# Kernel optimization log

Hardware: AMD Instinct MI355X
Metric: run time of the kernel (lower is better)

Reference implementation:

```python
import jax, jax.numpy as jnp
import numpy as np

N = 100000      # nodes
E = 1600000     # edges
IN_DIM = 256
HID = 64
NCLS = 32


def setup_inputs() -> dict:
    key = jax.random.key(0)
    ks = jax.random.split(key, 7)
    features = jax.random.normal(ks[0], (N, IN_DIM), dtype=jnp.float32)
    hidden_prev = jax.random.normal(ks[1], (N, HID), dtype=jnp.float32)
    adj_indices = jax.random.randint(ks[2], (2, E), 0, N, dtype=jnp.int32)
    # torch.rand init, scaled by 0.1 to keep activations numerically sane
    W0 = jax.random.uniform(ks[3], (IN_DIM, HID), dtype=jnp.float32) * 0.1
    W1 = jax.random.uniform(ks[4], (HID, HID), dtype=jnp.float32) * 0.1
    W2 = jax.random.uniform(ks[5], (HID, NCLS), dtype=jnp.float32) * 0.1
    att_w = jax.random.uniform(ks[6], (2 * HID, 1), dtype=jnp.float32) * 0.1
    return {"features": features, "hidden_prev": hidden_prev,
            "adj_indices": adj_indices, "W0": W0, "W1": W1, "W2": W2,
            "att_w": att_w}


def _edge_softmax(scores, rows, n):
    # sparse softmax over dim=1 of an NxN COO: normalize per source row
    m = jax.ops.segment_max(scores, rows, num_segments=n)
    ex = jnp.exp(scores - m[rows])
    s = jax.ops.segment_sum(ex, rows, num_segments=n)
    return ex / s[rows]


def _compute_attention(hfeat, adj_indices, att_w):
    src, dst = adj_indices[0], adj_indices[1]
    h = hfeat.shape[1]
    # cat(f_src, f_dst) @ att_w == f_src @ w_a + f_dst @ w_b ; project per-node
    proj_a = hfeat @ att_w[:h, 0]   # [N]
    proj_b = hfeat @ att_w[h:, 0]   # [N]
    scores = jax.nn.leaky_relu(proj_a[src] + proj_b[dst])  # [E]
    return _edge_softmax(scores, src, hfeat.shape[0])


def _spmm(att_vals, adj_indices, x):
    # out[i] = sum_{(i,j) in E} att * x[j]
    src, dst = adj_indices[0], adj_indices[1]
    return jax.ops.segment_sum(att_vals[:, None] * x[dst], src,
                               num_segments=x.shape[0])


def reference(features, hidden_prev, adj_indices, W0, W1, W2, att_w):
    att = _compute_attention(hidden_prev, adj_indices, att_w)  # [E]
    h = features
    for W in (W0, W1, W2):
        h = jax.nn.elu(_spmm(att, adj_indices, h @ W))
    return jax.nn.log_softmax(h, axis=1)
```

## Files before the change

kernel.cpp:

```cpp
#include <hip/hip_runtime.h>
#include <math.h>

#define HIDN 64
#define NCLS_K 32
#define INDIM 256
#define BSHIFT 7
#define MAXBUCK 1024
#define BUCK_CAP 4096
#define DSTBITS 17

typedef unsigned int uint;
typedef __attribute__((ext_vector_type(8))) short short8v;
typedef __attribute__((ext_vector_type(4))) float f32x4;

__device__ inline float bflo(uint u) { return __uint_as_float(u << 16); }
__device__ inline float bfhi(uint u) { return __uint_as_float(u & 0xFFFF0000u); }
__device__ inline unsigned short f2bf(float f) {
  uint u = __float_as_uint(f);
  return (unsigned short)((u + 0x7FFFu + ((u >> 16) & 1u)) >> 16);
}

__global__ __launch_bounds__(256) void proj_kernel(const float* __restrict__ hid,
    const float* __restrict__ attw, float* __restrict__ pa, float* __restrict__ pb, int n) {
  int wid  = (blockIdx.x * blockDim.x + threadIdx.x) >> 6;
  int lane = threadIdx.x & 63;
  if (wid >= n) return;
  float v = hid[(size_t)wid * HIDN + lane];
  float a = v * attw[lane];
  float b = v * attw[HIDN + lane];
  #pragma unroll
  for (int off = 32; off >= 1; off >>= 1) {
    a += __shfl_xor(a, off, 64);
    b += __shfl_xor(b, off, 64);
  }
  if (lane == 0) { pa[wid] = a; pb[wid] = b; }
}

__global__ __launch_bounds__(256) void hist_kernel(const int* __restrict__ src,
    int* __restrict__ bcnt, int e, int nb) {
  __shared__ int h[MAXBUCK];
  for (int j = threadIdx.x; j < MAXBUCK; j += 256) h[j] = 0;
  __syncthreads();
  for (int i = blockIdx.x * 256 + threadIdx.x; i < e; i += gridDim.x * 256)
    atomicAdd(&h[src[i] >> BSHIFT], 1);
  __syncthreads();
  for (int j = threadIdx.x; j < nb; j += 256)
    if (h[j]) atomicAdd(&bcnt[j], h[j]);
}

__global__ __launch_bounds__(1024) void scan_buckets(const int* __restrict__ bcnt,
    int* __restrict__ bbase, int* __restrict__ rowp, int nb, int n, int e) {
  __shared__ int sm[1024];
  int tid = threadIdx.x;
  int v = (tid < nb) ? bcnt[tid] : 0;
  sm[tid] = v;
  __syncthreads();
  for (int off = 1; off < 1024; off <<= 1) {
    int t = (tid >= off) ? sm[tid - off] : 0;
    __syncthreads();
    sm[tid] += t;
    __syncthreads();
  }
  if (tid < nb) bbase[tid] = sm[tid] - v;
  if (tid == 0) { bbase[nb] = e; rowp[n] = e; }
}

__global__ __launch_bounds__(256) void scatter_pairs(const int* __restrict__ src,
    const int* __restrict__ dst, const int* __restrict__ bbase,
    int* __restrict__ bcur, int* __restrict__ pairs, int e, int nb) {
  __shared__ int h[MAXBUCK];
  int nper = (e + gridDim.x - 1) / gridDim.x;
  int lo = blockIdx.x * nper;
  int hi = min(e, lo + nper);
  for (int j = threadIdx.x; j < nb; j += 256) h[j] = 0;
  __syncthreads();
  for (int i = lo + threadIdx.x; i < hi; i += 256)
    atomicAdd(&h[src[i] >> BSHIFT], 1);
  __syncthreads();
  for (int j = threadIdx.x; j < nb; j += 256) {
    int c = h[j];
    h[j] = c ? (bbase[j] + atomicAdd(&bcur[j], c)) : 0;
  }
  __syncthreads();
  for (int i = lo + threadIdx.x; i < hi; i += 256) {
    int s = src[i];
    int pos = atomicAdd(&h[s >> BSHIFT], 1);
    pairs[pos] = ((s & 127) << DSTBITS) | dst[i];
  }
}

__global__ __launch_bounds__(256) void build_csr(const int* __restrict__ pairs,
    const int* __restrict__ bbase, int* __restrict__ rowp,
    int* __restrict__ dstc, int n) {
  __shared__ int hist[128];
  __shared__ int cur[128];
  __shared__ int ord[BUCK_CAP];
  int b = blockIdx.x;
  int tid = threadIdx.x;
  int base = bbase[b];
  int m = bbase[b + 1] - base;
  if (tid < 128) hist[tid] = 0;
  __syncthreads();
  for (int i = tid; i < m; i += 256)
    atomicAdd(&hist[pairs[base + i] >> DSTBITS], 1);
  __syncthreads();
  int own = (tid < 128) ? hist[tid] : 0;
  for (int off = 1; off < 128; off <<= 1) {
    int t = (tid < 128 && tid >= off) ? hist[tid - off] : 0;
    __syncthreads();
    if (tid < 128) hist[tid] += t;
    __syncthreads();
  }
  if (tid < 128) {
    int excl = hist[tid] - own;
    cur[tid] = excl;
    int s = (b << BSHIFT) + tid;
    if (s < n) rowp[s] = base + excl;
  }
  __syncthreads();
  for (int i = tid; i < m; i += 256) {
    int key = pairs[base + i];
    int pos = atomicAdd(&cur[key >> DSTBITS], 1);
    ord[pos] = key & ((1 << DSTBITS) - 1);
  }
  __syncthreads();
  for (int i = tid; i < m; i += 256) dstc[base + i] = ord[i];
}

__device__ inline int wave_sort64(int key, int lane) {
  #pragma unroll
  for (int k = 2; k <= 64; k <<= 1) {
    #pragma unroll
    for (int j = k >> 1; j > 0; j >>= 1) {
      int p = __shfl_xor(key, j, 64);
      bool up    = ((lane & k) == 0);
      bool lower = ((lane & j) == 0);
      int mn = min(key, p), mx = max(key, p);
      key = (lower == up) ? mn : mx;
    }
  }
  return key;
}

__global__ __launch_bounds__(256) void att_softmax(const float* __restrict__ pa,
    const float* __restrict__ pb, int* __restrict__ dstc,
    const int* __restrict__ rowp, float* __restrict__ attv, int n) {
  int wid  = (blockIdx.x * blockDim.x + threadIdx.x) >> 6;
  int lane = threadIdx.x & 63;
  if (wid >= n) return;
  int start = rowp[wid], end = rowp[wid + 1];
  int c = end - start;
  if (c <= 0) return;
  float pai = pa[wid];
  if (c <= 64) {
    int e = start + lane;
    int key = (lane < c) ? dstc[e] : 0x7FFFFFFF;
    key = wave_sort64(key, lane);
    float s = -3.0e38f;
    if (lane < c) {
      dstc[e] = key;
      float v = pai + pb[key];
      s = v > 0.f ? v : 0.01f * v;
    }
    float m = s;
    #pragma unroll
    for (int off = 32; off >= 1; off >>= 1) m = fmaxf(m, __shfl_xor(m, off, 64));
    float ex = (lane < c) ? expf(s - m) : 0.f;
    float sum = ex;
    #pragma unroll
    for (int off = 32; off >= 1; off >>= 1) sum += __shfl_xor(sum, off, 64);
    if (lane < c) attv[e] = ex / sum;
    return;
  }
  float m = -3.0e38f;
  for (int base = start; base < end; base += 64) {
    int e = base + lane;
    int key = (e < end) ? dstc[e] : 0x7FFFFFFF;
    key = wave_sort64(key, lane);
    float s = -3.0e38f;
    if (e < end) {
      dstc[e] = key;
      float v = pai + pb[key];
      s = v > 0.f ? v : 0.01f * v;
      attv[e] = s;
    }
    m = fmaxf(m, s);
  }
  #pragma unroll
  for (int off = 32; off >= 1; off >>= 1) m = fmaxf(m, __shfl_xor(m, off, 64));
  float sum = 0.f;
  for (int base = start; base < end; base += 64) {
    int e = base + lane;
    float ex = 0.f;
    if (e < end) { ex = expf(attv[e] - m); attv[e] = ex; }
    sum += ex;
  }
  #pragma unroll
  for (int off = 32; off >= 1; off >>= 1) sum += __shfl_xor(sum, off, 64);
  float inv = 1.f / sum;
  for (int base = start; base < end; base += 64) {
    int e = base + lane;
    if (e < end) attv[e] *= inv;
  }
}

template <int K, int TJ>
__global__ __launch_bounds__(256) void gemm_mfma(const float* __restrict__ A,
    const float* __restrict__ W, unsigned short* __restrict__ Xb, int n) {
  constexpr int KP = K + 8;
  constexpr int NCB = TJ / 16;
  __shared__ unsigned short Wt[TJ][KP];
  const int tid = threadIdx.x;
  for (int idx = tid; idx < K * TJ; idx += 256) {
    int k = idx / TJ, j = idx % TJ;
    Wt[j][k] = f2bf(W[idx]);
  }
  __syncthreads();
  const int wv   = blockIdx.x * 4 + (tid >> 6);
  const int row0 = wv * 16;
  if (row0 >= n) return;
  const int lane = tid & 63;
  const int r    = lane & 15;
  const int kg   = lane >> 4;
  const int rowA = min(row0 + r, n - 1);
  const float* ap = A + (size_t)rowA * K + kg * 8;

  f32x4 acc[NCB];
  #pragma unroll
  for (int c = 0; c < NCB; ++c) acc[c] = (f32x4)(0.f);

  #pragma unroll
  for (int ks = 0; ks < K / 32; ++ks) {
    float4 a0 = *reinterpret_cast<const float4*>(ap + ks * 32);
    float4 a1 = *reinterpret_cast<const float4*>(ap + ks * 32 + 4);
    union { short8v v; unsigned short u[8]; } af;
    af.u[0] = f2bf(a0.x); af.u[1] = f2bf(a0.y);
    af.u[2] = f2bf(a0.z); af.u[3] = f2bf(a0.w);
    af.u[4] = f2bf(a1.x); af.u[5] = f2bf(a1.y);
    af.u[6] = f2bf(a1.z); af.u[7] = f2bf(a1.w);
    #pragma unroll
    for (int c = 0; c < NCB; ++c) {
      short8v bf = *reinterpret_cast<const short8v*>(&Wt[c * 16 + r][ks * 32 + kg * 8]);
      acc[c] = __builtin_amdgcn_mfma_f32_16x16x32_bf16(af.v, bf, acc[c], 0, 0, 0);
    }
  }
  #pragma unroll
  for (int c = 0; c < NCB; ++c) {
    #pragma unroll
    for (int i = 0; i < 4; ++i) {
      int rowS = row0 + kg * 4 + i;
      if (rowS < n) Xb[(size_t)rowS * TJ + c * 16 + r] = f2bf(acc[c][i]);
    }
  }
}

template <int J, bool FINAL>
__global__ __launch_bounds__(256) void spmm_elu(const uint4* __restrict__ Xv,
    const float* __restrict__ attv, const int* __restrict__ dstc,
    const int* __restrict__ rowp, float* __restrict__ out, int n) {
  constexpr int GW  = J / 8;
  constexpr int EPW = 64 / GW;
  int wid  = (blockIdx.x * blockDim.x + threadIdx.x) >> 6;
  int lane = threadIdx.x & 63;
  if (wid >= n) return;
  int start = rowp[wid], end = rowp[wid + 1];
  int g    = lane & (GW - 1);
  int esub = lane / GW;
  float a0[8], a1[8];
  #pragma unroll
  for (int k = 0; k < 8; ++k) { a0[k] = 0.f; a1[k] = 0.f; }
  for (int base = start; base < end; base += 64) {
    int e = base + lane;
    float av = 0.f; int dv = 0;
    if (e < end) { av = attv[e]; dv = dstc[e]; }
    int cnt = min(64, end - base);
    for (int t = 0; t < cnt; t += 2 * EPW) {
      {
        int mi = t + esub;
        float bv = __shfl(av, mi);
        int   d  = __shfl(dv, mi);
        uint4 u = Xv[(size_t)d * GW + g];
        a0[0] += bv * bflo(u.x); a0[1] += bv * bfhi(u.x);
        a0[2] += bv * bflo(u.y); a0[3] += bv * bfhi(u.y);
        a0[4] += bv * bflo(u.z); a0[5] += bv * bfhi(u.z);
        a0[6] += bv * bflo(u.w); a0[7] += bv * bfhi(u.w);
      }
      {
        int mi = t + EPW + esub;
        float bv = __shfl(av, mi);
        int   d  = __shfl(dv, mi);
        uint4 u = Xv[(size_t)d * GW + g];
        a1[0] += bv * bflo(u.x); a1[1] += bv * bfhi(u.x);
        a1[2] += bv * bflo(u.y); a1[3] += bv * bfhi(u.y);
        a1[4] += bv * bflo(u.z); a1[5] += bv * bfhi(u.z);
        a1[6] += bv * bflo(u.w); a1[7] += bv * bfhi(u.w);
      }
    }
  }
  float acc[8];
  #pragma unroll
  for (int k = 0; k < 8; ++k) acc[k] = a0[k] + a1[k];
  #pragma unroll
  for (int off = GW; off < 64; off <<= 1)
    #pragma unroll
    for (int k = 0; k < 8; ++k) acc[k] += __shfl_xor(acc[k], off);
  #pragma unroll
  for (int k = 0; k < 8; ++k)
    acc[k] = acc[k] > 0.f ? acc[k] : (expf(acc[k]) - 1.f);
  if (!FINAL) {
    if (lane < GW) {
      float* op = out + (size_t)wid * J + lane * 8;
      *reinterpret_cast<float4*>(op)     = make_float4(acc[0], acc[1], acc[2], acc[3]);
      *reinterpret_cast<float4*>(op + 4) = make_float4(acc[4], acc[5], acc[6], acc[7]);
    }
  } else {
    float m = acc[0];
    #pragma unroll
    for (int k = 1; k < 8; ++k) m = fmaxf(m, acc[k]);
    #pragma unroll
    for (int off = 1; off < GW; off <<= 1) m = fmaxf(m, __shfl_xor(m, off));
    float s = 0.f;
    #pragma unroll
    for (int k = 0; k < 8; ++k) s += expf(acc[k] - m);
    #pragma unroll
    for (int off = 1; off < GW; off <<= 1) s += __shfl_xor(s, off);
    float lg = m + logf(s);
    if (lane < GW) {
      float* op = out + (size_t)wid * J + lane * 8;
      *reinterpret_cast<float4*>(op)     = make_float4(acc[0] - lg, acc[1] - lg,
                                                       acc[2] - lg, acc[3] - lg);
      *reinterpret_cast<float4*>(op + 4) = make_float4(acc[4] - lg, acc[5] - lg,
                                                       acc[6] - lg, acc[7] - lg);
    }
  }
}

extern "C" void kernel_launch(void* const* d_in, const int* in_sizes, int n_in,
                              void* d_out, int out_size, void* d_ws, size_t ws_size,
                              hipStream_t stream) {
  const float* features = (const float*)d_in[0];
  const float* hidden   = (const float*)d_in[1];
  const int*   adj      = (const int*)d_in[2];
  const float* W0       = (const float*)d_in[3];
  const float* W1       = (const float*)d_in[4];
  const float* W2       = (const float*)d_in[5];
  const float* attw     = (const float*)d_in[6];
  float* out = (float*)d_out;

  const int N = in_sizes[1] / HIDN;
  const int E = in_sizes[2] / 2;
  const int* src = adj;
  const int* dst = adj + E;
  const int NBUCK = (N + 127) >> BSHIFT;
  const int NB2   = ((NBUCK + 15) / 16) * 16;

  int*   rowp  = (int*)d_ws;
  int*   bbase = rowp + (N + 16);
  int*   bcnt  = bbase + (NB2 + 16);
  int*   bcur  = bcnt + NB2;
  int*   dstc  = bcur + NB2;
  float* attv  = (float*)(dstc + E);
  float* Xf    = attv + E;
  float* H     = Xf + (size_t)N * HIDN;
  unsigned short* Xb = (unsigned short*)Xf;
  int*   pairs = (int*)Xf;
  float* pa    = H;
  float* pb    = H + N;

  (void)hipMemsetAsync(bcnt, 0, (size_t)2 * NB2 * sizeof(int), stream);

  dim3 blk(256);
  const int gridWave = (N + 3) / 4;
  const int gridGemm = ((N + 15) / 16 + 3) / 4;

  proj_kernel<<<gridWave, blk, 0, stream>>>(hidden, attw, pa, pb, N);
  hist_kernel<<<512, blk, 0, stream>>>(src, bcnt, E, NBUCK);
  scan_buckets<<<1, 1024, 0, stream>>>(bcnt, bbase, rowp, NBUCK, N, E);
  scatter_pairs<<<128, blk, 0, stream>>>(src, dst, bbase, bcur, pairs, E, NBUCK);
  build_csr<<<NBUCK, blk, 0, stream>>>(pairs, bbase, rowp, dstc, N);
  att_softmax<<<gridWave, blk, 0, stream>>>(pa, pb, dstc, rowp, attv, N);

  gemm_mfma<INDIM, HIDN><<<gridGemm, blk, 0, stream>>>(features, W0, Xb, N);
  spmm_elu<HIDN, false><<<gridWave, blk, 0, stream>>>(
      (const uint4*)Xb, attv, dstc, rowp, H, N);
  gemm_mfma<HIDN, HIDN><<<gridGemm, blk, 0, stream>>>(H, W1, Xb, N);
  spmm_elu<HIDN, false><<<gridWave, blk, 0, stream>>>(
      (const uint4*)Xb, attv, dstc, rowp, H, N);
  gemm_mfma<HIDN, NCLS_K><<<gridGemm, blk, 0, stream>>>(H, W2, Xb, N);
  spmm_elu<NCLS_K, true><<<gridWave, blk, 0, stream>>>(
      (const uint4*)Xb, attv, dstc, rowp, out, N);
}
```

Before: 333.0 us.

## Compute sparse aggregation with MFMA over 16-row tiles and bf16 attention

Replaces the per-row wave SpMM with a kernel where each wave handles 16 destination rows and feeds 32 edges per step into a bf16 MFMA. The attention operand is masked by the row id packed into the high bits of dstc, and the edge gather is done per column lane. Attention weights are stored as bf16 to halve their traffic. This trades vectorised 16-byte gathers for scalar 2-byte gathers and mostly-zero MFMA operands, and it loses precision in the attention values.

```diff
diff --git a/kernel.cpp b/kernel.cpp
--- a/kernel.cpp
+++ b/kernel.cpp
@@ -8,17 +8,20 @@
 #define MAXBUCK 1024
 #define BUCK_CAP 4096
 #define DSTBITS 17
+#define DSTMASK ((1 << DSTBITS) - 1)
 
 typedef unsigned int uint;
+typedef unsigned short ushort;
 typedef __attribute__((ext_vector_type(8))) short short8v;
 typedef __attribute__((ext_vector_type(4))) float f32x4;
 
 __device__ inline float bflo(uint u) { return __uint_as_float(u << 16); }
 __device__ inline float bfhi(uint u) { return __uint_as_float(u & 0xFFFF0000u); }
-__device__ inline unsigned short f2bf(float f) {
+__device__ inline ushort f2bf(float f) {
   uint u = __float_as_uint(f);
-  return (unsigned short)((u + 0x7FFFu + ((u >> 16) & 1u)) >> 16);
-}
+  return (ushort)((u + 0x7FFFu + ((u >> 16) & 1u)) >> 16);
+}
+__device__ inline float bf2f(ushort h) { return __uint_as_float(((uint)h) << 16); }
 
 __global__ __launch_bounds__(256) void proj_kernel(const float* __restrict__ hid,
     const float* __restrict__ attw, float* __restrict__ pa, float* __restrict__ pb, int n) {
@@ -121,7 +124,7 @@
   for (int i = tid; i < m; i += 256) {
     int key = pairs[base + i];
     int pos = atomicAdd(&cur[key >> DSTBITS], 1);
-    ord[pos] = key & ((1 << DSTBITS) - 1);
+    ord[pos] = key;
   }
   __syncthreads();
   for (int i = tid; i < m; i += 256) dstc[base + i] = ord[i];
@@ -144,7 +147,7 @@
 
 __global__ __launch_bounds__(256) void att_softmax(const float* __restrict__ pa,
     const float* __restrict__ pb, int* __restrict__ dstc,
-    const int* __restrict__ rowp, float* __restrict__ attv, int n) {
+    const int* __restrict__ rowp, ushort* __restrict__ attb, int n) {
   int wid  = (blockIdx.x * blockDim.x + threadIdx.x) >> 6;
   int lane = threadIdx.x & 63;
   if (wid >= n) return;
@@ -159,7 +162,7 @@
     float s = -3.0e38f;
     if (lane < c) {
       dstc[e] = key;
-      float v = pai + pb[key];
+      float v = pai + pb[key & DSTMASK];
       s = v > 0.f ? v : 0.01f * v;
     }
     float m = s;
@@ -169,7 +172,7 @@
     float sum = ex;
     #pragma unroll
     for (int off = 32; off >= 1; off >>= 1) sum += __shfl_xor(sum, off, 64);
-    if (lane < c) attv[e] = ex / sum;
+    if (lane < c) attb[e] = f2bf(ex / sum);
     return;
   }
   float m = -3.0e38f;
@@ -180,9 +183,9 @@
     float s = -3.0e38f;
     if (e < end) {
       dstc[e] = key;
-      float v = pai + pb[key];
+      float v = pai + pb[key & DSTMASK];
       s = v > 0.f ? v : 0.01f * v;
-      attv[e] = s;
+      attb[e] = f2bf(s);
     }
     m = fmaxf(m, s);
   }
@@ -192,7 +195,7 @@
   for (int base = start; base < end; base += 64) {
     int e = base + lane;
     float ex = 0.f;
-    if (e < end) { ex = expf(attv[e] - m); attv[e] = ex; }
+    if (e < end) { ex = expf(bf2f(attb[e]) - m); attb[e] = f2bf(ex); }
     sum += ex;
   }
   #pragma unroll
@@ -200,16 +203,16 @@
   float inv = 1.f / sum;
   for (int base = start; base < end; base += 64) {
     int e = base + lane;
-    if (e < end) attv[e] *= inv;
+    if (e < end) attb[e] = f2bf(bf2f(attb[e]) * inv);
   }
 }
 
 template <int K, int TJ>
 __global__ __launch_bounds__(256) void gemm_mfma(const float* __restrict__ A,
-    const float* __restrict__ W, unsigned short* __restrict__ Xb, int n) {
+    const float* __restrict__ W, ushort* __restrict__ Xb, int n) {
   constexpr int KP = K + 8;
   constexpr int NCB = TJ / 16;
-  __shared__ unsigned short Wt[TJ][KP];
+  __shared__ ushort Wt[TJ][KP];
   const int tid = threadIdx.x;
   for (int idx = tid; idx < K * TJ; idx += 256) {
     int k = idx / TJ, j = idx % TJ;
@@ -233,7 +236,7 @@
   for (int ks = 0; ks < K / 32; ++ks) {
     float4 a0 = *reinterpret_cast<const float4*>(ap + ks * 32);
     float4 a1 = *reinterpret_cast<const float4*>(ap + ks * 32 + 4);
-    union { short8v v; unsigned short u[8]; } af;
+    union { short8v v; ushort u[8]; } af;
     af.u[0] = f2bf(a0.x); af.u[1] = f2bf(a0.y);
     af.u[2] = f2bf(a0.z); af.u[3] = f2bf(a0.w);
     af.u[4] = f2bf(a1.x); af.u[5] = f2bf(a1.y);
@@ -254,83 +257,82 @@
   }
 }
 
-template <int J, bool FINAL>
-__global__ __launch_bounds__(256) void spmm_elu(const uint4* __restrict__ Xv,
-    const float* __restrict__ attv, const int* __restrict__ dstc,
+template <int TJ, bool FINAL>
+__global__ __launch_bounds__(256) void spmm_mfma(const ushort* __restrict__ Xb,
+    const ushort* __restrict__ attb, const int* __restrict__ dstc,
     const int* __restrict__ rowp, float* __restrict__ out, int n) {
-  constexpr int GW  = J / 8;
-  constexpr int EPW = 64 / GW;
-  int wid  = (blockIdx.x * blockDim.x + threadIdx.x) >> 6;
-  int lane = threadIdx.x & 63;
-  if (wid >= n) return;
-  int start = rowp[wid], end = rowp[wid + 1];
-  int g    = lane & (GW - 1);
-  int esub = lane / GW;
-  float a0[8], a1[8];
-  #pragma unroll
-  for (int k = 0; k < 8; ++k) { a0[k] = 0.f; a1[k] = 0.f; }
-  for (int base = start; base < end; base += 64) {
-    int e = base + lane;
-    float av = 0.f; int dv = 0;
-    if (e < end) { av = attv[e]; dv = dstc[e]; }
-    int cnt = min(64, end - base);
-    for (int t = 0; t < cnt; t += 2 * EPW) {
-      {
-        int mi = t + esub;
-        float bv = __shfl(av, mi);
-        int   d  = __shfl(dv, mi);
-        uint4 u = Xv[(size_t)d * GW + g];
-        a0[0] += bv * bflo(u.x); a0[1] += bv * bfhi(u.x);
-        a0[2] += bv * bflo(u.y); a0[3] += bv * bfhi(u.y);
-        a0[4] += bv * bflo(u.z); a0[5] += bv * bfhi(u.z);
-        a0[6] += bv * bflo(u.w); a0[7] += bv * bfhi(u.w);
+  constexpr int NCB = TJ / 16;
+  const int tid  = threadIdx.x;
+  const int g    = blockIdx.x * 4 + (tid >> 6);
+  const int row0 = g * 16;
+  if (row0 >= n) return;
+  const int lane = tid & 63;
+  const int r    = lane & 15;
+  const int kg   = lane >> 4;
+  const int start = rowp[row0];
+  const int end   = rowp[min(row0 + 16, n)];
+
+  f32x4 acc[NCB];
+  #pragma unroll
+  for (int c = 0; c < NCB; ++c) acc[c] = (f32x4)(0.f);
+
+  for (int base = start; base < end; base += 32) {
+    int sbase = base + 8 * kg;
+    union { short8v v; ushort u[8]; } af;
+    int dv[8];
+    #pragma unroll
+    for (int j = 0; j < 8; ++j) {
+      int e = sbase + j;
+      bool valid = e < end;
+      int idx = valid ? e : (end - 1);
+      int v = dstc[idx];
+      ushort a = attb[idx];
+      int rid = (v >> DSTBITS) & 15;
+      af.u[j] = (valid && rid == r) ? a : (ushort)0;
+      dv[j] = v & DSTMASK;
+    }
+    #pragma unroll
+    for (int c = 0; c < NCB; ++c) {
+      union { short8v v; ushort u[8]; } bf;
+      #pragma unroll
+      for (int j = 0; j < 8; ++j)
+        bf.u[j] = Xb[(size_t)dv[j] * TJ + c * 16 + r];
+      acc[c] = __builtin_amdgcn_mfma_f32_16x16x32_bf16(af.v, bf.v, acc[c], 0, 0, 0);
+    }
+  }
+  #pragma unroll
+  for (int c = 0; c < NCB; ++c)
+    #pragma unroll
+    for (int i = 0; i < 4; ++i)
+      acc[c][i] = acc[c][i] > 0.f ? acc[c][i] : (expf(acc[c][i]) - 1.f);
+  if (!FINAL) {
+    #pragma unroll
+    for (int c = 0; c < NCB; ++c)
+      #pragma unroll
+      for (int i = 0; i < 4; ++i) {
+        int rowS = row0 + kg * 4 + i;
+        if (rowS < n) out[(size_t)rowS * TJ + c * 16 + r] = acc[c][i];
       }
-      {
-        int mi = t + EPW + esub;
-        float bv = __shfl(av, mi);
-        int   d  = __shfl(dv, mi);
-        uint4 u = Xv[(size_t)d * GW + g];
-        a1[0] += bv * bflo(u.x); a1[1] += bv * bfhi(u.x);
-        a1[2] += bv * bflo(u.y); a1[3] += bv * bfhi(u.y);
-        a1[4] += bv * bflo(u.z); a1[5] += bv * bfhi(u.z);
-        a1[6] += bv * bflo(u.w); a1[7] += bv * bfhi(u.w);
+  } else {
+    #pragma unroll
+    for (int i = 0; i < 4; ++i) {
+      float m = acc[0][i];
+      #pragma unroll
+      for (int c = 1; c < NCB; ++c) m = fmaxf(m, acc[c][i]);
+      #pragma unroll
+      for (int off = 1; off < 16; off <<= 1) m = fmaxf(m, __shfl_xor(m, off));
+      float s = 0.f;
+      #pragma unroll
+      for (int c = 0; c < NCB; ++c) s += expf(acc[c][i] - m);
+      #pragma unroll
+      for (int off = 1; off < 16; off <<= 1) s += __shfl_xor(s, off);
+      float lg = m + logf(s);
+      int rowS = row0 + kg * 4 + i;
+      if (rowS < n) {
+        #pragma unroll
+        for (int c = 0; c < NCB; ++c)
+          out[(size_t)rowS * TJ + c * 16 + r] = acc[c][i] - lg;
       }
-    }
-  }
-  float acc[8];
-  #pragma unroll
-  for (int k = 0; k < 8; ++k) acc[k] = a0[k] + a1[k];
-  #pragma unroll
-  for (int off = GW; off < 64; off <<= 1)
-    #pragma unroll
-    for (int k = 0; k < 8; ++k) acc[k] += __shfl_xor(acc[k], off);
-  #pragma unroll
-  for (int k = 0; k < 8; ++k)
-    acc[k] = acc[k] > 0.f ? acc[k] : (expf(acc[k]) - 1.f);
-  if (!FINAL) {
-    if (lane < GW) {
-      float* op = out + (size_t)wid * J + lane * 8;
-      *reinterpret_cast<float4*>(op)     = make_float4(acc[0], acc[1], acc[2], acc[3]);
-      *reinterpret_cast<float4*>(op + 4) = make_float4(acc[4], acc[5], acc[6], acc[7]);
-    }
-  } else {
-    float m = acc[0];
-    #pragma unroll
-    for (int k = 1; k < 8; ++k) m = fmaxf(m, acc[k]);
-    #pragma unroll
-    for (int off = 1; off < GW; off <<= 1) m = fmaxf(m, __shfl_xor(m, off));
-    float s = 0.f;
-    #pragma unroll
-    for (int k = 0; k < 8; ++k) s += expf(acc[k] - m);
-    #pragma unroll
-    for (int off = 1; off < GW; off <<= 1) s += __shfl_xor(s, off);
-    float lg = m + logf(s);
-    if (lane < GW) {
-      float* op = out + (size_t)wid * J + lane * 8;
-      *reinterpret_cast<float4*>(op)     = make_float4(acc[0] - lg, acc[1] - lg,
-                                                       acc[2] - lg, acc[3] - lg);
-      *reinterpret_cast<float4*>(op + 4) = make_float4(acc[4] - lg, acc[5] - lg,
-                                                       acc[6] - lg, acc[7] - lg);
     }
   }
 }
@@ -359,10 +361,10 @@
   int*   bcnt  = bbase + (NB2 + 16);
   int*   bcur  = bcnt + NB2;
   int*   dstc  = bcur + NB2;
-  float* attv  = (float*)(dstc + E);
-  float* Xf    = attv + E;
+  ushort* attb = (ushort*)(dstc + E);
+  float* Xf    = (float*)(attb) + (E / 2 + 16);
   float* H     = Xf + (size_t)N * HIDN;
-  unsigned short* Xb = (unsigned short*)Xf;
+  ushort* Xb   = (ushort*)Xf;
   int*   pairs = (int*)Xf;
   float* pa    = H;
   float* pb    = H + N;
@@ -371,22 +373,19 @@
 
   dim3 blk(256);
   const int gridWave = (N + 3) / 4;
-  const int gridGemm = ((N + 15) / 16 + 3) / 4;
+  const int gridG16  = ((N + 15) / 16 + 3) / 4;
 
   proj_kernel<<<gridWave, blk, 0, stream>>>(hidden, attw, pa, pb, N);
   hist_kernel<<<512, blk, 0, stream>>>(src, bcnt, E, NBUCK);
   scan_buckets<<<1, 1024, 0, stream>>>(bcnt, bbase, rowp, NBUCK, N, E);
   scatter_pairs<<<128, blk, 0, stream>>>(src, dst, bbase, bcur, pairs, E, NBUCK);
   build_csr<<<NBUCK, blk, 0, stream>>>(pairs, bbase, rowp, dstc, N);
-  att_softmax<<<gridWave, blk, 0, stream>>>(pa, pb, dstc, rowp, attv, N);
-
-  gemm_mfma<INDIM, HIDN><<<gridGemm, blk, 0, stream>>>(features, W0, Xb, N);
-  spmm_elu<HIDN, false><<<gridWave, blk, 0, stream>>>(
-      (const uint4*)Xb, attv, dstc, rowp, H, N);
-  gemm_mfma<HIDN, HIDN><<<gridGemm, blk, 0, stream>>>(H, W1, Xb, N);
-  spmm_elu<HIDN, false><<<gridWave, blk, 0, stream>>>(
-      (const uint4*)Xb, attv, dstc, rowp, H, N);
-  gemm_mfma<HIDN, NCLS_K><<<gridGemm, blk, 0, stream>>>(H, W2, Xb, N);
-  spmm_elu<NCLS_K, true><<<gridWave, blk, 0, stream>>>(
-      (const uint4*)Xb, attv, dstc, rowp, out, N);
-}
+  att_softmax<<<gridWave, blk, 0, stream>>>(pa, pb, dstc, rowp, attb, N);
+
+  gemm_mfma<INDIM, HIDN><<<gridG16, blk, 0, stream>>>(features, W0, Xb, N);
+  spmm_mfma<HIDN, false><<<gridG16, blk, 0, stream>>>(Xb, attb, dstc, rowp, H, N);
+  gemm_mfma<HIDN, HIDN><<<gridG16, blk, 0, stream>>>(H, W1, Xb, N);
+  spmm_mfma<HIDN, false><<<gridG16, blk, 0, stream>>>(Xb, attb, dstc, rowp, H, N);
+  gemm_mfma<HIDN, NCLS_K><<<gridG16, blk, 0, stream>>>(H, W2, Xb, N);
+  spmm_mfma<NCLS_K, true><<<gridG16, blk, 0, stream>>>(Xb, attb, dstc, rowp, out, N);
+}
```

After: 325.1 us. 2.4% less time.
